# Optimization experiments

Measured on AMD Instinct MI355X. Metric: run time of the kernel, lower is better.

## Reference

```python
import jax, jax.numpy as jnp
import numpy as np

# Module hyperparameters (from init_kwargs)
H, F = 8, 32            # num_heads, attention_filters
RY, RX = 3, 3           # spatial_radius
PH, PW = 2 * RY + 1, 2 * RX + 1
S = PH * PW             # patch_size = 49
HF = H * F


def setup_inputs() -> dict:
    key = jax.random.key(0)
    ks = jax.random.split(key, 6)
    B, Y, X, C = 4, 64, 64, 256
    x = jax.random.normal(ks[0], (B, Y, X, C), jnp.float32)
    # 1x1 conv kernels == dense matrices over the channel dim (no bias)
    Wq = jax.random.normal(ks[1], (C, HF), jnp.float32) / np.sqrt(C)
    Wk = jax.random.normal(ks[2], (C, HF), jnp.float32) / np.sqrt(C)
    Wv = jax.random.normal(ks[3], (C, HF), jnp.float32) / np.sqrt(C)
    Wo = jax.random.normal(ks[4], (HF, C), jnp.float32) / np.sqrt(HF)
    pos_emb = jax.random.normal(ks[5], (S, HF), jnp.float32) * 0.02
    return {"x": x, "Wq": Wq, "Wk": Wk, "Wv": Wv, "Wo": Wo, "pos_emb": pos_emb}


def reference(x, Wq, Wk, Wv, Wo, pos_emb):
    B, Y, X, C = x.shape
    dtype = x.dtype
    # 1x1 conv projections
    Q = x @ Wq                       # (B,Y,X,HF)
    K = x @ Wk
    V = x @ Wv
    # clipped patch centers (borders reuse interior patches)
    cy = jnp.clip(jnp.arange(Y), RY, Y - RY - 1)   # (Y,)
    cx = jnp.clip(jnp.arange(X), RX, X - RX - 1)   # (X,)
    # query relative-position indices within its patch
    qy = jnp.arange(Y) - cy + RY
    qx = jnp.arange(X) - cx + RX
    qidx = qy[:, None] * PW + qx[None, :]          # (Y,X) in [0,S)
    Q = Q + pos_emb[qidx]                          # add query pos embedding (HF)
    Q = Q.reshape(B, Y, X, H, F)
    K = K.reshape(B, Y, X, H, F)
    V = V.reshape(B, Y, X, H, F)
    cy_g, cx_g = jnp.meshgrid(cy, cx, indexing="ij")  # (Y,X)
    scale = jnp.asarray(1.0 / np.sqrt(F), dtype)
    NEG = jnp.asarray(-1e9, dtype)
    m = jnp.full((B, Y, X, H, 1), NEG, dtype)      # running max
    l = jnp.zeros((B, Y, X, H, 1), dtype)          # running sum-exp
    acc = jnp.zeros((B, Y, X, H, F), dtype)        # running value accumulator
    dy_vec = np.arange(-RY, RY + 1)                # within-chunk offsets ('col' mode)
    for dx in range(-RX, RX + 1):                  # chunk loop over columns (7 chunks)
        ny = jnp.clip(cy_g[None, :, :] + dy_vec[:, None, None], 0, Y - 1)  # (PH,Y,X)
        nx = jnp.clip(cx_g[None, :, :] + dx, 0, X - 1)                     # (1,Y,X)
        nx = jnp.broadcast_to(nx, ny.shape)
        sidx = (dy_vec + RY) * PW + (dx + RX)      # (PH,) relative-pos indices
        # gather neighbor K/V: (B,PH,Y,X,H,F)
        Kc = K[:, ny, nx] + pos_emb[sidx].reshape(PH, 1, 1, H, F)
        Vc = V[:, ny, nx]
        sc = jnp.einsum("byxhf,bsyxhf->byxhs", Q, Kc) * scale  # (B,Y,X,H,PH)
        new_m = jnp.maximum(m, sc.max(axis=-1, keepdims=True))
        alpha = jnp.exp(m - new_m)
        p = jnp.exp(sc - new_m)
        l = l * alpha + p.sum(axis=-1, keepdims=True)
        acc = acc * alpha + jnp.einsum("byxhs,bsyxhf->byxhf", p, Vc)
        m = new_m
    out = (acc / (l + 1e-8)).reshape(B, Y, X, HF) @ Wo
    return out
```

## Files before the change

### kernel.cpp

```cpp
#include <hip/hip_runtime.h>
#include <hip/hip_bf16.h>

static constexpr int NPOS = 4 * 64 * 64;
static constexpr int CD   = 256;
#define QSCALE (0.17677669529663687f * 1.4426950408889634f)

typedef __attribute__((ext_vector_type(8))) short bf16x8;
typedef __attribute__((ext_vector_type(4))) float f32x4;

__device__ __forceinline__ float bf2f(unsigned short u) {
    return __uint_as_float((unsigned int)u << 16);
}
__device__ __forceinline__ unsigned short bfbits(float f) {
    union { __hip_bfloat16 h; unsigned short u; } cv;
    cv.h = __float2bfloat16(f);
    return cv.u;
}
__device__ __forceinline__ unsigned int packbf2(float lo, float hi) {
    union { __hip_bfloat162 h; unsigned int u; } cv;
    cv.h.x = __float2bfloat16(lo);
    cv.h.y = __float2bfloat16(hi);
    return cv.u;
}
__device__ __forceinline__ uint4 pack8(float4 a, float4 b) {
    uint4 u;
    u.x = packbf2(a.x, a.y); u.y = packbf2(a.z, a.w);
    u.z = packbf2(b.x, b.y); u.w = packbf2(b.z, b.w);
    return u;
}
template<int CTRL>
__device__ __forceinline__ float dpp_mov(float v) {
    return __int_as_float(
        __builtin_amdgcn_update_dpp(0, __float_as_int(v), CTRL, 0xF, 0xF, true));
}
template<int IMM>
__device__ __forceinline__ float swz(float v) {
    return __int_as_float(__builtin_amdgcn_ds_swizzle(__float_as_int(v), IMM));
}

__global__ __launch_bounds__(256) void convert_kernel(
    const float* __restrict__ Wq, const float* __restrict__ Wk,
    const float* __restrict__ Wv, const float* __restrict__ Wo,
    const float* __restrict__ pe,
    __hip_bfloat16* __restrict__ Wfrag,
    __hip_bfloat16* __restrict__ pebf,
    __hip_bfloat16* __restrict__ Wofrag)
{
    int t = blockIdx.x * 256 + threadIdx.x;
    if (t < 24576) {
        int L = t & 63, ng = (t >> 6) & 7, s = (t >> 9) & 7, T = t >> 12;
        int mat = T >> 1;
        const float* src = (mat == 0) ? Wq : (mat == 1) ? Wk : Wv;
        int ncol  = (T & 1) * 128 + ng * 16 + (L & 15);
        int kbase = s * 32 + (L >> 4) * 8;
        __hip_bfloat16* dst = Wfrag + ((size_t)((T * 8 + s) * 8 + ng) * 64 + L) * 8;
#pragma unroll
        for (int j = 0; j < 8; ++j)
            dst[j] = __float2bfloat16(src[(kbase + j) * 256 + ncol]);
    } else if (t < 26624) {
        int u = t - 24576;
        int L = u & 63, Tn = (u >> 6) & 3, h = u >> 8;
        int s = Tn * 16 + (L & 15);
        int kbase = (L >> 4) * 8;
        __hip_bfloat16* dst = pebf + ((size_t)((h * 4 + Tn) * 64 + L)) * 8;
#pragma unroll
        for (int j = 0; j < 8; ++j) {
            float v = (s < 49) ? pe[s * 256 + h * 32 + kbase + j] * QSCALE : 0.f;
            dst[j] = __float2bfloat16(v);
        }
    } else if (t < 34816) {
        int u = t - 26624;
        int L = u & 63, ng = (u >> 6) & 7, s = (u >> 9) & 7, T = (u >> 12) & 1;
        int ncol  = T * 128 + ng * 16 + (L & 15);
        int kbase = s * 32 + (L >> 4) * 8;
        __hip_bfloat16* dst = Wofrag + ((size_t)((T * 8 + s) * 8 + ng) * 64 + L) * 8;
#pragma unroll
        for (int j = 0; j < 8; ++j)
            dst[j] = __float2bfloat16(Wo[(kbase + j) * 256 + ncol]);
    }
}

__global__ __launch_bounds__(256, 4) void qkv_mfma(
    const float* __restrict__ x,
    const __hip_bfloat16* __restrict__ Wfrag,
    const float* __restrict__ pe,
    unsigned short* __restrict__ QA,
    unsigned short* __restrict__ Kd,
    unsigned short* __restrict__ Vt)
{
    __shared__ __align__(16) unsigned short smem[256 * 68];
    short* As0 = (short*)smem;
    short* As1 = As0 + 2048;
    const int t = threadIdx.x;
    const int rowbase = blockIdx.x * 64;
    const int g = blockIdx.y;
    const int L = t & 63;
    const int wave = t >> 6;
    const int quad = L >> 4, lrow = L & 15;
    const int T = g * 2 + (wave >> 1);
    const int ngb = (wave & 1) * 4;

    f32x4 acc[4][4];
#pragma unroll
    for (int i = 0; i < 4; ++i)
#pragma unroll
        for (int j = 0; j < 4; ++j) acc[i][j] = (f32x4){0.f, 0.f, 0.f, 0.f};

    const float* xsrc = x + (size_t)(rowbase + (t >> 2)) * CD + (t & 3) * 8;
    const __hip_bfloat16* wbase = Wfrag + ((size_t)(T * 8 * 8 + ngb) * 64 + L) * 8;

    float4 f0 = ((const float4*)xsrc)[0];
    float4 f1 = ((const float4*)xsrc)[1];
    ((uint4*)As0)[t] = pack8(f0, f1);
    f0 = ((const float4*)(xsrc + 32))[0];
    f1 = ((const float4*)(xsrc + 32))[1];

    bf16x8 bfr[4];
#pragma unroll
    for (int j = 0; j < 4; ++j)
        bfr[j] = *(const bf16x8*)(wbase + (size_t)j * 64 * 8);
    __syncthreads();

#pragma unroll
    for (int s = 0; s < 8; ++s) {
        bf16x8 nbfr[4];
        if (s < 7) {
#pragma unroll
            for (int j = 0; j < 4; ++j)
                nbfr[j] = *(const bf16x8*)(wbase + (size_t)((s + 1) * 8 + j) * 64 * 8);
        }
        if (s < 7) {
            ((uint4*)((s & 1) ? As0 : As1))[t] = pack8(f0, f1);
            if (s < 6) {
                f0 = ((const float4*)(xsrc + (s + 2) * 32))[0];
                f1 = ((const float4*)(xsrc + (s + 2) * 32))[1];
            }
        }
        const short* Ab = (s & 1) ? As1 : As0;
#pragma unroll
        for (int i = 0; i < 4; ++i) {
            bf16x8 af = *(const bf16x8*)(Ab + (i * 16 + lrow) * 32 + quad * 8);
#pragma unroll
            for (int j = 0; j < 4; ++j)
                acc[i][j] = __builtin_amdgcn_mfma_f32_16x16x32_bf16(af, bfr[j], acc[i][j], 0, 0, 0);
        }
        __syncthreads();
#pragma unroll
        for (int j = 0; j < 4; ++j) bfr[j] = nbfr[j];
    }

    if (g == 0) {
#pragma unroll
        for (int i = 0; i < 4; ++i)
#pragma unroll
            for (int r = 0; r < 4; ++r) {
                int row = rowbase + i * 16 + quad * 4 + r;
                int yy = (row >> 6) & 63, xx = row & 63;
                int cy = min(max(yy, 3), 60), cx = min(max(xx, 3), 60);
                int qidx = (yy - cy + 3) * 7 + (xx - cx + 3);
#pragma unroll
                for (int j = 0; j < 4; ++j) {
                    int c = wave * 64 + j * 16 + lrow;
                    QA[(size_t)row * CD + c] = bfbits(acc[i][j][r] + pe[qidx * 256 + c]);
                }
            }
    } else if (g == 1) {
#pragma unroll
        for (int i = 0; i < 4; ++i)
#pragma unroll
            for (int r = 0; r < 4; ++r) {
                int row = rowbase + i * 16 + quad * 4 + r;
#pragma unroll
                for (int j = 0; j < 4; ++j) {
                    int c = wave * 64 + j * 16 + lrow;
                    Kd[(size_t)row * CD + c] = bfbits(acc[i][j][r] * QSCALE);
                }
            }
    } else {
        unsigned short* vt = smem;
#pragma unroll
        for (int i = 0; i < 4; ++i)
#pragma unroll
            for (int j = 0; j < 4; ++j) {
                int c = wave * 64 + j * 16 + lrow;
                int row0 = i * 16 + quad * 4;
                *(unsigned int*)&vt[c * 68 + row0] =
                    (unsigned int)bfbits(acc[i][j][0]) | ((unsigned int)bfbits(acc[i][j][1]) << 16);
                *(unsigned int*)&vt[c * 68 + row0 + 2] =
                    (unsigned int)bfbits(acc[i][j][2]) | ((unsigned int)bfbits(acc[i][j][3]) << 16);
            }
        __syncthreads();
        const int grp = t >> 4, lig = t & 15;
        const int row_off = lig * 4;
#pragma unroll
        for (int pass = 0; pass < 16; ++pass) {
            int c = pass * 16 + grp;
            *(ushort4*)(Vt + (size_t)c * 16384 + rowbase + row_off) =
                *(const ushort4*)&vt[c * 68 + row_off];
        }
    }
}

__global__ __launch_bounds__(512) void attn_oproj(
    const unsigned short* __restrict__ QA,
    const unsigned short* __restrict__ Kd,
    const unsigned short* __restrict__ Vt,
    const __hip_bfloat16* __restrict__ pebf,
    const __hip_bfloat16* __restrict__ Wofrag,
    float* __restrict__ out)
{
    __shared__ unsigned short qpes[8][16 * 64];
    __shared__ __align__(16) unsigned short ps[8][16 * 40];
    __shared__ __align__(16) unsigned short At[16 * 264];
    const int t = threadIdx.x, w = t >> 6, L = t & 63;
    const int lrow = L & 15, quad = L >> 4;
    const int bid = blockIdx.x;
    const int tile = ((bid & 7) << 7) | (bid >> 3);
    const int pos0 = tile * 16;
    const int x0 = pos0 & 63;
    const int yy = (pos0 >> 6) & 63, bb = pos0 >> 12;
    const int cy = min(max(yy, 3), 60);
    const int h = w;

    const int kc0 = min(max(x0 - 8 + lrow, 0), 63);
    const int kc1 = min(max(x0 + 8 + lrow, 0), 63);
    const f32x4 zero = {0.f, 0.f, 0.f, 0.f};
    unsigned short* qp = qpes[w];
    unsigned short* pw = ps[w];

    int qi0[4], qi1[4];
    float mk0[4], mk1[4];
#pragma unroll
    for (int r = 0; r < 4; ++r) {
        const int i = quad * 4 + r;
        const int cxr = min(max(x0 + i, 3), 60) - x0 + 5;
        int dx3a = lrow - cxr;
        qi0[r] = i * 64 + min(max(dx3a, 0), 6);
        mk0[r] = ((unsigned)dx3a <= 6u) ? 1.f : 0.f;
        int dx3b = 16 + lrow - cxr;
        qi1[r] = i * 64 + min(max(dx3b, 0), 6);
        mk1[r] = ((unsigned)dx3b <= 6u) ? 1.f : 0.f;
    }

    const bf16x8 qa = *(const bf16x8*)(QA + (size_t)(pos0 + lrow) * 256 + h * 32 + quad * 8);

#pragma unroll
    for (int Tn = 0; Tn < 4; ++Tn) {
        bf16x8 bp = *(const bf16x8*)(pebf + ((size_t)((h * 4 + Tn) * 64 + L)) * 8);
        f32x4 c = __builtin_amdgcn_mfma_f32_16x16x32_bf16(qa, bp, zero, 0, 0, 0);
#pragma unroll
        for (int r = 0; r < 4; ++r)
            qp[(quad * 4 + r) * 64 + Tn * 16 + lrow] = bfbits(c[r]);
    }
    __builtin_amdgcn_s_waitcnt(0xc07f);

    float lacc[4] = {0.f, 0.f, 0.f, 0.f};
    f32x4 o0 = zero, o1 = zero;
    int rowpos = bb * 4096 + (cy - 3) * 64;

    const size_t koff = h * 32 + quad * 8;
    const size_t voff0 = (size_t)(h * 32 + lrow) * 16384 + x0 - 8 + quad * 8;
    const size_t voff1 = (size_t)(h * 32 + 16 + lrow) * 16384 + x0 - 8 + quad * 8;
    bf16x8 bk0 = *(const bf16x8*)(Kd + (size_t)(rowpos + kc0) * 256 + koff);
    bf16x8 bk1 = *(const bf16x8*)(Kd + (size_t)(rowpos + kc1) * 256 + koff);
    bf16x8 bv0 = *(const bf16x8*)(Vt + voff0 + rowpos);
    bf16x8 bv1 = *(const bf16x8*)(Vt + voff1 + rowpos);

    int qpofs = 0;
    for (int dy = 0; dy < 7; ++dy) {
        const int rnext = rowpos + 64;
        bf16x8 nk0, nk1, nv0, nv1;
        if (dy < 6) {
            nk0 = *(const bf16x8*)(Kd + (size_t)(rnext + kc0) * 256 + koff);
            nk1 = *(const bf16x8*)(Kd + (size_t)(rnext + kc1) * 256 + koff);
            nv0 = *(const bf16x8*)(Vt + voff0 + rnext);
            nv1 = *(const bf16x8*)(Vt + voff1 + rnext);
        }
        f32x4 sc0 = __builtin_amdgcn_mfma_f32_16x16x32_bf16(qa, bk0, zero, 0, 0, 0);
        f32x4 sc1 = __builtin_amdgcn_mfma_f32_16x16x32_bf16(qa, bk1, zero, 0, 0, 0);
#pragma unroll
        for (int r = 0; r < 4; ++r) {
            float e0 = exp2f(sc0[r] + bf2f(qp[qi0[r] + qpofs])) * mk0[r];
            lacc[r] += e0;
            pw[(quad * 4 + r) * 40 + lrow] = bfbits(e0);
            float e1 = exp2f(sc1[r] + bf2f(qp[qi1[r] + qpofs])) * mk1[r];
            lacc[r] += e1;
            pw[(quad * 4 + r) * 40 + 16 + lrow] = bfbits(e1);
        }
        __builtin_amdgcn_s_waitcnt(0xc07f);
        const bf16x8 pa = *(const bf16x8*)(pw + lrow * 40 + quad * 8);
        o0 = __builtin_amdgcn_mfma_f32_16x16x32_bf16(pa, bv0, o0, 0, 0, 0);
        o1 = __builtin_amdgcn_mfma_f32_16x16x32_bf16(pa, bv1, o1, 0, 0, 0);
        bk0 = nk0; bk1 = nk1; bv0 = nv0; bv1 = nv1;
        rowpos = rnext;
        qpofs += 7;
    }

#pragma unroll
    for (int r = 0; r < 4; ++r) {
        float v = lacc[r];
        v += dpp_mov<0xB1>(v);
        v += dpp_mov<0x4E>(v);
        v += swz<0x101F>(v);
        v += swz<0x201F>(v);
        const float inv = 1.f / (v + 1e-8f);
        const int arow = quad * 4 + r;
        At[arow * 264 + h * 32 + lrow]      = bfbits(o0[r] * inv);
        At[arow * 264 + h * 32 + 16 + lrow] = bfbits(o1[r] * inv);
    }
    __syncthreads();

    const int T = w >> 2;
    const int ngb = (w & 3) * 2;
    f32x4 acc[2];
    acc[0] = zero; acc[1] = zero;

#pragma unroll
    for (int s = 0; s < 8; ++s) {
        bf16x8 bfr[2];
#pragma unroll
        for (int j = 0; j < 2; ++j)
            bfr[j] = *(const bf16x8*)(Wofrag +
                      ((size_t)((T * 8 + s) * 8 + ngb + j) * 64 + L) * 8);
        bf16x8 af = *(const bf16x8*)(At + lrow * 264 + s * 32 + quad * 8);
#pragma unroll
        for (int j = 0; j < 2; ++j)
            acc[j] = __builtin_amdgcn_mfma_f32_16x16x32_bf16(af, bfr[j], acc[j], 0, 0, 0);
    }

#pragma unroll
    for (int r = 0; r < 4; ++r) {
        int row = pos0 + quad * 4 + r;
#pragma unroll
        for (int j = 0; j < 2; ++j) {
            int c = w * 32 + j * 16 + lrow;
            out[(size_t)row * CD + c] = acc[j][r];
        }
    }
}

extern "C" void kernel_launch(void* const* d_in, const int* in_sizes, int n_in,
                              void* d_out, int out_size, void* d_ws, size_t ws_size,
                              hipStream_t stream)
{
    const float* x  = (const float*)d_in[0];
    const float* Wq = (const float*)d_in[1];
    const float* Wk = (const float*)d_in[2];
    const float* Wv = (const float*)d_in[3];
    const float* Wo = (const float*)d_in[4];
    const float* pe = (const float*)d_in[5];
    float* out = (float*)d_out;

    char* ws = (char*)d_ws;
    unsigned short* QA = (unsigned short*)ws;
    unsigned short* Kd = (unsigned short*)(ws + (8u << 20));
    unsigned short* Vt = (unsigned short*)(ws + (16u << 20));
    char* fr = ws + (24u << 20) + 4096;
    __hip_bfloat16* Wfrag  = (__hip_bfloat16*)fr;
    __hip_bfloat16* pebf   = (__hip_bfloat16*)(fr + (384u << 10));
    __hip_bfloat16* Wofrag = (__hip_bfloat16*)(fr + (416u << 10));

    convert_kernel<<<136, 256, 0, stream>>>(Wq, Wk, Wv, Wo, pe, Wfrag, pebf, Wofrag);
    qkv_mfma<<<dim3(256, 3), 256, 0, stream>>>(x, Wfrag, pe, QA, Kd, Vt);
    attn_oproj<<<1024, 512, 0, stream>>>(QA, Kd, Vt, pebf, Wofrag, out);
}
```

Baseline: 122.8 us.

## Transpose attention MFMAs and pass probabilities via permlane swaps instead of LDS

The score and PV MFMAs are computed in transposed form (K/V as the A operand, Q/P as B), so each lane holds a query's scores along the key dimension. The softmax probabilities are repacked into the B-operand layout with permlane32/permlane16 swaps instead of being written to and re-read from a per-wave LDS buffer. This removes the ps shared buffer, its waitcnt, and the per-row cross-lane sum reductions, at the cost of new index math for the query positional terms. It also widens the qpes rows to 72 with packed 32-bit writes.

```diff
diff --git a/kernel.cpp b/kernel.cpp
--- a/kernel.cpp
+++ b/kernel.cpp
@@ -28,14 +28,13 @@
     u.z = packbf2(b.x, b.y); u.w = packbf2(b.z, b.w);
     return u;
 }
-template<int CTRL>
-__device__ __forceinline__ float dpp_mov(float v) {
-    return __int_as_float(
-        __builtin_amdgcn_update_dpp(0, __float_as_int(v), CTRL, 0xF, 0xF, true));
-}
-template<int IMM>
-__device__ __forceinline__ float swz(float v) {
-    return __int_as_float(__builtin_amdgcn_ds_swizzle(__float_as_int(v), IMM));
+__device__ __forceinline__ void pl32swap(unsigned &a, unsigned &b) {
+    auto r = __builtin_amdgcn_permlane32_swap(a, b, false, false);
+    a = r[0]; b = r[1];
+}
+__device__ __forceinline__ void pl16swap(unsigned &a, unsigned &b) {
+    auto r = __builtin_amdgcn_permlane16_swap(a, b, false, false);
+    a = r[0]; b = r[1];
 }
 
 __global__ __launch_bounds__(256) void convert_kernel(
@@ -209,8 +208,7 @@
     const __hip_bfloat16* __restrict__ Wofrag,
     float* __restrict__ out)
 {
-    __shared__ unsigned short qpes[8][16 * 64];
-    __shared__ __align__(16) unsigned short ps[8][16 * 40];
+    __shared__ __align__(16) unsigned short qpes[8][16 * 72];
     __shared__ __align__(16) unsigned short At[16 * 264];
     const int t = threadIdx.x, w = t >> 6, L = t & 63;
     const int lrow = L & 15, quad = L >> 4;
@@ -226,20 +224,19 @@
     const int kc1 = min(max(x0 + 8 + lrow, 0), 63);
     const f32x4 zero = {0.f, 0.f, 0.f, 0.f};
     unsigned short* qp = qpes[w];
-    unsigned short* pw = ps[w];
-
-    int qi0[4], qi1[4];
-    float mk0[4], mk1[4];
+
+    const int cx = min(max(x0 + lrow, 3), 60) - x0 + 5;
+    int qiA[4], qiB[4];
+    float mkA[4], mkB[4];
 #pragma unroll
     for (int r = 0; r < 4; ++r) {
-        const int i = quad * 4 + r;
-        const int cxr = min(max(x0 + i, 3), 60) - x0 + 5;
-        int dx3a = lrow - cxr;
-        qi0[r] = i * 64 + min(max(dx3a, 0), 6);
-        mk0[r] = ((unsigned)dx3a <= 6u) ? 1.f : 0.f;
-        int dx3b = 16 + lrow - cxr;
-        qi1[r] = i * 64 + min(max(dx3b, 0), 6);
-        mk1[r] = ((unsigned)dx3b <= 6u) ? 1.f : 0.f;
+        const int sl = quad * 4 + r;
+        int dxa = sl - cx;
+        qiA[r] = lrow * 72 + min(max(dxa, 0), 6);
+        mkA[r] = ((unsigned)dxa <= 6u) ? 1.f : 0.f;
+        int dxb = 16 + sl - cx;
+        qiB[r] = lrow * 72 + min(max(dxb, 0), 6);
+        mkB[r] = ((unsigned)dxb <= 6u) ? 1.f : 0.f;
     }
 
     const bf16x8 qa = *(const bf16x8*)(QA + (size_t)(pos0 + lrow) * 256 + h * 32 + quad * 8);
@@ -247,15 +244,14 @@
 #pragma unroll
     for (int Tn = 0; Tn < 4; ++Tn) {
         bf16x8 bp = *(const bf16x8*)(pebf + ((size_t)((h * 4 + Tn) * 64 + L)) * 8);
-        f32x4 c = __builtin_amdgcn_mfma_f32_16x16x32_bf16(qa, bp, zero, 0, 0, 0);
-#pragma unroll
-        for (int r = 0; r < 4; ++r)
-            qp[(quad * 4 + r) * 64 + Tn * 16 + lrow] = bfbits(c[r]);
+        f32x4 c = __builtin_amdgcn_mfma_f32_16x16x32_bf16(bp, qa, zero, 0, 0, 0);
+        *(unsigned int*)&qp[lrow * 72 + Tn * 16 + quad * 4]     = packbf2(c[0], c[1]);
+        *(unsigned int*)&qp[lrow * 72 + Tn * 16 + quad * 4 + 2] = packbf2(c[2], c[3]);
     }
     __builtin_amdgcn_s_waitcnt(0xc07f);
 
-    float lacc[4] = {0.f, 0.f, 0.f, 0.f};
-    f32x4 o0 = zero, o1 = zero;
+    float lacc = 0.f;
+    f32x4 oT0 = zero, oT1 = zero;
     int rowpos = bb * 4096 + (cy - 3) * 64;
 
     const size_t koff = h * 32 + quad * 8;
@@ -276,37 +272,44 @@
             nv0 = *(const bf16x8*)(Vt + voff0 + rnext);
             nv1 = *(const bf16x8*)(Vt + voff1 + rnext);
         }
-        f32x4 sc0 = __builtin_amdgcn_mfma_f32_16x16x32_bf16(qa, bk0, zero, 0, 0, 0);
-        f32x4 sc1 = __builtin_amdgcn_mfma_f32_16x16x32_bf16(qa, bk1, zero, 0, 0, 0);
-#pragma unroll
-        for (int r = 0; r < 4; ++r) {
-            float e0 = exp2f(sc0[r] + bf2f(qp[qi0[r] + qpofs])) * mk0[r];
-            lacc[r] += e0;
-            pw[(quad * 4 + r) * 40 + lrow] = bfbits(e0);
-            float e1 = exp2f(sc1[r] + bf2f(qp[qi1[r] + qpofs])) * mk1[r];
-            lacc[r] += e1;
-            pw[(quad * 4 + r) * 40 + 16 + lrow] = bfbits(e1);
-        }
-        __builtin_amdgcn_s_waitcnt(0xc07f);
-        const bf16x8 pa = *(const bf16x8*)(pw + lrow * 40 + quad * 8);
-        o0 = __builtin_amdgcn_mfma_f32_16x16x32_bf16(pa, bv0, o0, 0, 0, 0);
-        o1 = __builtin_amdgcn_mfma_f32_16x16x32_bf16(pa, bv1, o1, 0, 0, 0);
+        f32x4 s0 = __builtin_amdgcn_mfma_f32_16x16x32_bf16(bk0, qa, zero, 0, 0, 0);
+        f32x4 s1 = __builtin_amdgcn_mfma_f32_16x16x32_bf16(bk1, qa, zero, 0, 0, 0);
+        float e00 = exp2f(s0[0] + bf2f(qp[qiA[0] + qpofs])) * mkA[0];
+        float e01 = exp2f(s0[1] + bf2f(qp[qiA[1] + qpofs])) * mkA[1];
+        float e02 = exp2f(s0[2] + bf2f(qp[qiA[2] + qpofs])) * mkA[2];
+        float e03 = exp2f(s0[3] + bf2f(qp[qiA[3] + qpofs])) * mkA[3];
+        float e10 = exp2f(s1[0] + bf2f(qp[qiB[0] + qpofs])) * mkB[0];
+        float e11 = exp2f(s1[1] + bf2f(qp[qiB[1] + qpofs])) * mkB[1];
+        float e12 = exp2f(s1[2] + bf2f(qp[qiB[2] + qpofs])) * mkB[2];
+        float e13 = exp2f(s1[3] + bf2f(qp[qiB[3] + qpofs])) * mkB[3];
+        lacc += ((e00 + e01) + (e02 + e03)) + ((e10 + e11) + (e12 + e13));
+
+        unsigned p0 = packbf2(e00, e01), p1 = packbf2(e02, e03);
+        unsigned z0 = packbf2(e10, e11), z1 = packbf2(e12, e13);
+        pl32swap(p0, z0);
+        pl16swap(p0, z0);
+        pl32swap(p1, z1);
+        pl16swap(p1, z1);
+        union { unsigned u[4]; bf16x8 v; } pb;
+        pb.u[0] = p0; pb.u[1] = p1; pb.u[2] = z0; pb.u[3] = z1;
+
+        oT0 = __builtin_amdgcn_mfma_f32_16x16x32_bf16(bv0, pb.v, oT0, 0, 0, 0);
+        oT1 = __builtin_amdgcn_mfma_f32_16x16x32_bf16(bv1, pb.v, oT1, 0, 0, 0);
         bk0 = nk0; bk1 = nk1; bv0 = nv0; bv1 = nv1;
         rowpos = rnext;
         qpofs += 7;
     }
 
-#pragma unroll
-    for (int r = 0; r < 4; ++r) {
-        float v = lacc[r];
-        v += dpp_mov<0xB1>(v);
-        v += dpp_mov<0x4E>(v);
-        v += swz<0x101F>(v);
-        v += swz<0x201F>(v);
-        const float inv = 1.f / (v + 1e-8f);
-        const int arow = quad * 4 + r;
-        At[arow * 264 + h * 32 + lrow]      = bfbits(o0[r] * inv);
-        At[arow * 264 + h * 32 + 16 + lrow] = bfbits(o1[r] * inv);
+    lacc += __shfl_xor(lacc, 16);
+    lacc += __shfl_xor(lacc, 32);
+    const float inv = 1.f / (lacc + 1e-8f);
+
+    {
+        const int base = lrow * 264 + h * 32 + quad * 4;
+        *(unsigned int*)&At[base]          = packbf2(oT0[0] * inv, oT0[1] * inv);
+        *(unsigned int*)&At[base + 2]      = packbf2(oT0[2] * inv, oT0[3] * inv);
+        *(unsigned int*)&At[base + 16]     = packbf2(oT1[0] * inv, oT1[1] * inv);
+        *(unsigned int*)&At[base + 16 + 2] = packbf2(oT1[2] * inv, oT1[3] * inv);
     }
     __syncthreads();
 
```

New measurement: 124.8 us. About the same (+1.6%).
